# Optimization experiments

Measured on AMD Instinct MI355X. Metric: run time of the kernel, lower is better.

The kernel has to match this reference:

```python
import jax, jax.numpy as jnp
import numpy as np

N = 50000      # nodes
E = 800000     # edges (avg degree 16)
IN = 128       # in_feats
HID = 32       # hidden_feats per head
H = 4          # num_heads
NEG_SLOPE = 0.2


def setup_inputs() -> dict:
    key = jax.random.key(0)
    ks = jax.random.split(key, 13)
    x = jax.random.normal(ks[0], (N, IN), jnp.float32)
    src = jax.random.randint(ks[1], (E,), 0, N, jnp.int32)
    dst = jax.random.randint(ks[2], (E,), 0, N, jnp.int32)

    def lin(k, fi, fo):
        return jax.random.normal(k, (fi, fo), jnp.float32) * (1.0 / np.sqrt(fi))

    # conv1: IN -> H*HID
    W1 = lin(ks[3], IN, H * HID)
    al1 = jax.random.normal(ks[4], (H, HID), jnp.float32) * 0.1
    ar1 = jax.random.normal(ks[5], (H, HID), jnp.float32) * 0.1
    b1 = jnp.zeros((H, HID), jnp.float32)
    # conv2: H*HID -> H*HID
    W2 = lin(ks[6], H * HID, H * HID)
    al2 = jax.random.normal(ks[7], (H, HID), jnp.float32) * 0.1
    ar2 = jax.random.normal(ks[8], (H, HID), jnp.float32) * 0.1
    b2 = jnp.zeros((H, HID), jnp.float32)
    # fc: HID -> 1
    fcW = lin(ks[9], HID, 1)
    fcb = jnp.zeros((1,), jnp.float32)
    return {"x": x, "src": src, "dst": dst,
            "W1": W1, "al1": al1, "ar1": ar1, "b1": b1,
            "W2": W2, "al2": al2, "ar2": ar2, "b2": b2,
            "fcW": fcW, "fcb": fcb}


def gat_conv(x, src, dst, W, al, ar, b):
    # x: [N, F_in] -> feat: [N, H, HID]
    feat = (x @ W).reshape(N, H, HID)
    el = jnp.sum(feat * al, axis=-1)            # [N, H]
    er = jnp.sum(feat * ar, axis=-1)            # [N, H]
    e = jax.nn.leaky_relu(el[src] + er[dst], NEG_SLOPE)  # [E, H]
    # segment softmax over incoming edges of each dst node
    m = jax.ops.segment_max(e, dst, num_segments=N)      # [N, H]
    ex = jnp.exp(e - m[dst])                              # [E, H]
    denom = jax.ops.segment_sum(ex, dst, num_segments=N)  # [N, H]
    alpha = ex / denom[dst]                                # [E, H]
    msg = feat[src] * alpha[:, :, None]                    # [E, H, HID]
    out = jax.ops.segment_sum(msg, dst, num_segments=N)   # [N, H, HID]
    return out + b[None, :, :]


def reference(x, src, dst, W1, al1, ar1, b1, W2, al2, ar2, b2, fcW, fcb):
    h = gat_conv(x, src, dst, W1, al1, ar1, b1).reshape(N, H * HID)
    h = jax.nn.relu(h)
    # dropout(0.5) is identity in eval mode
    h = gat_conv(h, src, dst, W2, al2, ar2, b2).mean(axis=1)  # [N, HID]
    return h @ fcW + fcb                                       # [N, 1]
```

## Files before the change

kernel.cpp:

```cpp
#include <hip/hip_runtime.h>
#include <hip/hip_fp16.h>

#define LEAK 0.2f
#define CAP 64

static __device__ inline unsigned pack_h2(float a, float b) {
    __half2 h = __floats2half2_rn(a, b);
    unsigned u; __builtin_memcpy(&u, &h, 4); return u;
}
static __device__ inline int swz(int c, int j) {
    int qb = j >> 3, r = j & 7;
    return c * 144 + qb * 8 + (qb >> 2) * 4 + r;
}
static __device__ inline unsigned q4(float4 v, float is) {
    int x0 = __float2int_rn(v.x * is) + 128; x0 = min(max(x0, 0), 255);
    int x1 = __float2int_rn(v.y * is) + 128; x1 = min(max(x1, 0), 255);
    int x2 = __float2int_rn(v.z * is) + 128; x2 = min(max(x2, 0), 255);
    int x3 = __float2int_rn(v.w * is) + 128; x3 = min(max(x3, 0), 255);
    return (unsigned)x0 | ((unsigned)x1 << 8) | ((unsigned)x2 << 16) | ((unsigned)x3 << 24);
}

__global__ __launch_bounds__(256, 4) void k1(
    const float* __restrict__ X, const float* __restrict__ W,
    const float* __restrict__ al, const float* __restrict__ ar,
    float2* __restrict__ elsc2, float* __restrict__ er_nh,
    unsigned* __restrict__ fq8,
    int* __restrict__ cnt,
    const float* __restrict__ W2, const float* __restrict__ al2,
    const float* __restrict__ ar2, const float* __restrict__ fcW,
    const float* __restrict__ b2, float* __restrict__ WfT,
    float* __restrict__ bc, int N, int ntiles, int zb) {
    __shared__ float sW[32 * 128];
    __shared__ float sXT[32 * 128];
    const int b = blockIdx.x;
    const int t = threadIdx.x;

    if (b >= ntiles) {
        int bb = b - ntiles;
        if (bb < zb) {
            int i = bb * 256 + t;
            if (i < N) cnt[i] = 0;
        } else {
            int idx = (bb - zb) * 256 + t;
            if (idx < 1536) {
                int c = idx >> 7, k = idx & 127;
                int h = c & 3, sel = c >> 2;
                const float* vec = (sel == 0) ? (al2 + 32 * h)
                                 : (sel == 1) ? (ar2 + 32 * h) : fcW;
                float s = 0.f;
#pragma unroll 8
                for (int m = 0; m < 32; m++) s += W2[k * 128 + 32 * h + m] * vec[m];
                WfT[c * 128 + k] = s;
            } else if (idx < 1540) {
                int h = idx - 1536;
                float s = 0.f;
                for (int m = 0; m < 32; m++) s += b2[h * 32 + m] * fcW[m];
                bc[h] = s;
            }
        }
        return;
    }

    const int r0 = b * 128;
    const int tx = t & 15;
    const int ty = t >> 4;
    const float4* X4 = (const float4*)X;
    const float4* W4 = (const float4*)W;
    float4* sW4 = (float4*)sW;
    const float4* sXT4 = (const float4*)sXT;

    float4 acc[8][2];
#pragma unroll
    for (int r = 0; r < 8; r++) {
        acc[r][0] = make_float4(0.f, 0.f, 0.f, 0.f);
        acc[r][1] = make_float4(0.f, 0.f, 0.f, 0.f);
    }
    for (int ks = 0; ks < 4; ++ks) {
        if (ks) __syncthreads();
#pragma unroll
        for (int i = 0; i < 4; i++) {
            int idx = i * 256 + t;
            sW4[idx] = W4[1024 * ks + idx];
        }
#pragma unroll
        for (int i = 0; i < 4; i++) {
            int idx = i * 256 + t;
            int row = idx >> 3;
            int kq = idx & 7;
            float4 v = make_float4(0.f, 0.f, 0.f, 0.f);
            if (r0 + row < N) v = X4[(size_t)(r0 + row) * 32 + ks * 8 + kq];
            int sc = (((row >> 2) ^ kq)) * 4 + (row & 3);
            sXT[(4 * kq + 0) * 128 + sc] = v.x;
            sXT[(4 * kq + 1) * 128 + sc] = v.y;
            sXT[(4 * kq + 2) * 128 + sc] = v.z;
            sXT[(4 * kq + 3) * 128 + sc] = v.w;
        }
        __syncthreads();
#pragma unroll 4
        for (int k = 0; k < 32; k++) {
            float4 w0 = sW4[k * 32 + tx];
            float4 w1 = sW4[k * 32 + 16 + tx];
            float4 x0 = sXT4[k * 32 + (ty ^ (k >> 2))];
            float4 x1 = sXT4[k * 32 + ((16 + ty) ^ (k >> 2))];
            float xs[8] = {x0.x, x0.y, x0.z, x0.w, x1.x, x1.y, x1.z, x1.w};
#pragma unroll
            for (int r = 0; r < 8; r++) {
                acc[r][0].x += xs[r] * w0.x; acc[r][0].y += xs[r] * w0.y;
                acc[r][0].z += xs[r] * w0.z; acc[r][0].w += xs[r] * w0.w;
                acc[r][1].x += xs[r] * w1.x; acc[r][1].y += xs[r] * w1.y;
                acc[r][1].z += xs[r] * w1.z; acc[r][1].w += xs[r] * w1.w;
            }
        }
    }
    const float4* al4p = (const float4*)al;
    const float4* ar4p = (const float4*)ar;
    float4 alA = al4p[tx], alB = al4p[16 + tx];
    float4 arA = ar4p[tx], arB = ar4p[16 + tx];
#pragma unroll
    for (int r = 0; r < 8; r++) {
        int lrow = (r < 4) ? (ty * 4 + r) : (64 + ty * 4 + (r - 4));
        int row = r0 + lrow;
        bool ok = row < N;
        float4 a0 = acc[r][0], a1 = acc[r][1];
        float m = fmaxf(fmaxf(fmaxf(fabsf(a0.x), fabsf(a0.y)),
                              fmaxf(fabsf(a0.z), fabsf(a0.w))),
                        fmaxf(fmaxf(fabsf(a1.x), fabsf(a1.y)),
                              fmaxf(fabsf(a1.z), fabsf(a1.w))));
#pragma unroll
        for (int off = 1; off < 16; off <<= 1) m = fmaxf(m, __shfl_xor(m, off));
        float scale = m * (1.f / 127.f);
        float is = (m > 0.f) ? (127.f / m) : 0.f;
        if (ok) {
            fq8[(size_t)row * 32 + tx] = q4(a0, is);
            fq8[(size_t)row * 32 + 16 + tx] = q4(a1, is);
        }
        float elA = a0.x * alA.x + a0.y * alA.y + a0.z * alA.z + a0.w * alA.w;
        float erA = a0.x * arA.x + a0.y * arA.y + a0.z * arA.z + a0.w * arA.w;
        float elB = a1.x * alB.x + a1.y * alB.y + a1.z * alB.z + a1.w * alB.w;
        float erB = a1.x * arB.x + a1.y * arB.y + a1.z * arB.z + a1.w * arB.w;
#pragma unroll
        for (int off = 1; off < 8; off <<= 1) {
            elA += __shfl_xor(elA, off); erA += __shfl_xor(erA, off);
            elB += __shfl_xor(elB, off); erB += __shfl_xor(erB, off);
        }
        if (ok && tx == 0) {
            elsc2[row * 4 + 0] = make_float2(elA, scale);
            elsc2[row * 4 + 2] = make_float2(elB, scale);
            er_nh[row * 4 + 0] = erA;
            er_nh[row * 4 + 2] = erB;
        }
        if (ok && tx == 8) {
            elsc2[row * 4 + 1] = make_float2(elA, scale);
            elsc2[row * 4 + 3] = make_float2(elB, scale);
            er_nh[row * 4 + 1] = erA;
            er_nh[row * 4 + 3] = erB;
        }
    }
}

__global__ __launch_bounds__(256) void k_ell(
    const int* __restrict__ src, const int* __restrict__ dst,
    int* __restrict__ cnt, unsigned short* __restrict__ ell,
    int E, int N, int R) {
    const int part = blockIdx.x & 7;
    const int rank = blockIdx.x >> 3;
    const int S = (N + 7) >> 3;
    const int lo = part * S;
    const int hi = (lo + S < N) ? (lo + S) : N;
    const int per = (E + R - 1) / R;
    const int e0 = rank * per;
    const int e1 = (e0 + per < E) ? (e0 + per) : E;
    for (int e = e0 + threadIdx.x; e < e1; e += 256) {
        int d = dst[e];
        if (d >= lo && d < hi) {
            int s = src[e];
            int pos = atomicAdd(&cnt[d], 1);
            if (pos < CAP) ell[(size_t)d * CAP + pos] = (unsigned short)s;
        }
    }
}

__global__ __launch_bounds__(256) void k_agg1P(
    const unsigned* __restrict__ fq8, const float2* __restrict__ elsc2,
    const float* __restrict__ er_nh, const unsigned short* __restrict__ ell,
    const int* __restrict__ cnt, const float* __restrict__ b1,
    const float* __restrict__ WfT, float2* __restrict__ Pag,
    float* __restrict__ er2, int N) {
    __shared__ float sWf[12 * 144];
    for (int i = threadIdx.x; i < 1536; i += 256)
        sWf[swz(i >> 7, i & 127)] = WfT[i];
    __syncthreads();
    const int wave = threadIdx.x >> 6, lane = threadIdx.x & 63;
    const int nsub = lane >> 4, q = lane & 15, h = q >> 2;
    const int wbase = q * 8 + (q >> 2) * 4;
    const uint2* fq2 = (const uint2*)fq8;

    const int n = blockIdx.x * 16 + wave * 4 + nsub;
    const bool nok = n < N;
    const int nc = nok ? n : (N - 1);
    int deg = nok ? cnt[n] : 0; if (deg > CAP) deg = CAP;
    float er = nok ? er_nh[n * 4 + h] : 0.f;
    const unsigned short* row = ell + (size_t)nc * CAP;

    int dm = deg;
    dm = max(dm, __shfl_xor(dm, 16));
    dm = max(dm, __shfl_xor(dm, 32));

    float acc[8] = {0.f, 0.f, 0.f, 0.f, 0.f, 0.f, 0.f, 0.f};
    float den = 0.f, wss = 0.f;
    for (int jt = 0; jt < dm; jt += 16) {
        int s_all = (jt + q < CAP) ? (int)row[jt + q] : 0;
        int lim = dm - jt; if (lim > 16) lim = 16;
        for (int u = 0; u < lim; u += 8) {
            int sv[8]; float2 esv[8]; uint2 fv[8];
#pragma unroll
            for (int v = 0; v < 8; v++) {
                int jj = jt + u + v;
                int s = __shfl(s_all, (lane & 48) | ((u + v) & 15));
                sv[v] = (jj < deg) ? s : 0;
            }
#pragma unroll
            for (int v = 0; v < 8; v++) esv[v] = elsc2[sv[v] * 4 + h];
#pragma unroll
            for (int v = 0; v < 8; v++) fv[v] = fq2[(size_t)sv[v] * 16 + q];
#pragma unroll
            for (int v = 0; v < 8; v++) {
                int jj = jt + u + v;
                bool valid = jj < deg;
                float e = esv[v].x + er;
                e = fmaxf(e, LEAK * e);
                float w = valid ? __expf(e) : 0.f;
                float ws = w * esv[v].y;
                unsigned ua = fv[v].x, ub = fv[v].y;
                acc[0] += ws * (float)(ua & 0xff);
                acc[1] += ws * (float)((ua >> 8) & 0xff);
                acc[2] += ws * (float)((ua >> 16) & 0xff);
                acc[3] += ws * (float)(ua >> 24);
                acc[4] += ws * (float)(ub & 0xff);
                acc[5] += ws * (float)((ub >> 8) & 0xff);
                acc[6] += ws * (float)((ub >> 16) & 0xff);
                acc[7] += ws * (float)(ub >> 24);
                den += w; wss += ws;
            }
        }
    }
    float inv = (den > 0.f) ? (1.f / den) : 0.f;
    float off128 = 128.f * wss;
    float4 b1a = ((const float4*)b1)[q * 2];
    float4 b1b = ((const float4*)b1)[q * 2 + 1];
    float hv[8];
    hv[0] = fmaxf((acc[0] - off128) * inv + b1a.x, 0.f);
    hv[1] = fmaxf((acc[1] - off128) * inv + b1a.y, 0.f);
    hv[2] = fmaxf((acc[2] - off128) * inv + b1a.z, 0.f);
    hv[3] = fmaxf((acc[3] - off128) * inv + b1a.w, 0.f);
    hv[4] = fmaxf((acc[4] - off128) * inv + b1b.x, 0.f);
    hv[5] = fmaxf((acc[5] - off128) * inv + b1b.y, 0.f);
    hv[6] = fmaxf((acc[6] - off128) * inv + b1b.z, 0.f);
    hv[7] = fmaxf((acc[7] - off128) * inv + b1b.w, 0.f);
    float p[12];
#pragma unroll
    for (int c = 0; c < 12; c++) {
        const float* wr = sWf + c * 144 + wbase;
        float4 wa = *(const float4*)wr;
        float4 wb = *(const float4*)(wr + 4);
        p[c] = hv[0] * wa.x + hv[1] * wa.y + hv[2] * wa.z + hv[3] * wa.w
             + hv[4] * wb.x + hv[5] * wb.y + hv[6] * wb.z + hv[7] * wb.w;
    }
#pragma unroll
    for (int off = 1; off < 16; off <<= 1) {
#pragma unroll
        for (int c = 0; c < 12; c++) p[c] += __shfl_xor(p[c], off);
    }
    if (nok) {
        if (q < 4) Pag[(size_t)n * 4 + q] = make_float2(p[q], p[8 + q]);
        else if (q < 8) er2[(size_t)n * 4 + (q - 4)] = p[q];
    }
}

__global__ __launch_bounds__(256) void k_agg2(
    const float2* __restrict__ Pag, const float* __restrict__ er2,
    const unsigned short* __restrict__ ell, const int* __restrict__ cnt,
    const float* __restrict__ bc, const float* __restrict__ fcb,
    float* __restrict__ out, int N) {
    int idx = blockIdx.x * 256 + threadIdx.x;
    int n = idx >> 2, h = idx & 3;
    if (n >= N) return;
    int deg = cnt[n]; if (deg > CAP) deg = CAP;
    float er = er2[(size_t)n * 4 + h];
    const unsigned short* row = ell + (size_t)n * CAP;
    float num = 0.f, den = 0.f;
    int j = 0, d4 = deg & ~3;
    for (; j < d4; j += 4) {
        ushort4 ss = *(const ushort4*)(row + j);
        int s0 = ss.x, s1 = ss.y, s2 = ss.z, s3 = ss.w;
        float2 g0 = Pag[(size_t)s0 * 4 + h];
        float2 g1 = Pag[(size_t)s1 * 4 + h];
        float2 g2 = Pag[(size_t)s2 * 4 + h];
        float2 g3 = Pag[(size_t)s3 * 4 + h];
        float e0 = g0.x + er; e0 = fmaxf(e0, LEAK * e0); float w0 = __expf(e0);
        float e1 = g1.x + er; e1 = fmaxf(e1, LEAK * e1); float w1 = __expf(e1);
        float e2 = g2.x + er; e2 = fmaxf(e2, LEAK * e2); float w2 = __expf(e2);
        float e3 = g3.x + er; e3 = fmaxf(e3, LEAK * e3); float w3 = __expf(e3);
        num += w0 * g0.y + w1 * g1.y + w2 * g2.y + w3 * g3.y;
        den += (w0 + w1) + (w2 + w3);
    }
    for (; j < deg; ++j) {
        int s = row[j];
        float2 gg = Pag[(size_t)s * 4 + h];
        float e = gg.x + er; e = fmaxf(e, LEAK * e);
        float w = __expf(e);
        num += w * gg.y; den += w;
    }
    float r = (den > 0.f) ? (num / den) : 0.f;
    r += bc[h];
    r += __shfl_xor(r, 1);
    r += __shfl_xor(r, 2);
    if (h == 0) out[n] = 0.25f * r + fcb[0];
}

extern "C" void kernel_launch(void* const* d_in, const int* in_sizes, int n_in,
                              void* d_out, int out_size, void* d_ws, size_t ws_size,
                              hipStream_t stream) {
    const float* x   = (const float*)d_in[0];
    const int* src   = (const int*)d_in[1];
    const int* dst   = (const int*)d_in[2];
    const float* W1  = (const float*)d_in[3];
    const float* al1 = (const float*)d_in[4];
    const float* ar1 = (const float*)d_in[5];
    const float* b1  = (const float*)d_in[6];
    const float* W2  = (const float*)d_in[7];
    const float* al2 = (const float*)d_in[8];
    const float* ar2 = (const float*)d_in[9];
    const float* b2  = (const float*)d_in[10];
    const float* fcW = (const float*)d_in[11];
    const float* fcb = (const float*)d_in[12];
    float* out = (float*)d_out;

    const int N = in_sizes[0] / 128;
    const int E = in_sizes[1];

    char* w = (char*)d_ws;
    size_t off = 0;
    auto alloc = [&](size_t bytes) {
        void* p = w + off;
        off = (off + bytes + 255) & ~(size_t)255;
        return p;
    };
    unsigned* fq8  = (unsigned*)alloc((size_t)N * 32 * 4);
    float2* elsc2  = (float2*)alloc((size_t)N * 4 * 8);
    float* er_nh   = (float*)alloc((size_t)N * 4 * 4);
    float2* Pag    = (float2*)alloc((size_t)N * 4 * 8);
    float* er2     = (float*)alloc((size_t)N * 4 * 4);
    float* WfT     = (float*)alloc((size_t)(12 * 128 + 4) * 4);
    float* bc      = WfT + 12 * 128;
    int* cnt       = (int*)alloc((size_t)N * 4);
    unsigned short* ell = (unsigned short*)alloc((size_t)N * CAP * 2);

    const int zb = (N + 255) / 256;
    const int ntiles = (N + 127) / 128;
    const int R = 256;

    k1<<<ntiles + zb + 8, 256, 0, stream>>>(
        x, W1, al1, ar1, elsc2, er_nh, fq8,
        cnt, W2, al2, ar2, fcW, b2, WfT, bc, N, ntiles, zb);
    k_ell<<<8 * R, 256, 0, stream>>>(src, dst, cnt, ell, E, N, R);
    k_agg1P<<<(N + 15) / 16, 256, 0, stream>>>(
        fq8, elsc2, er_nh, ell, cnt, b1, WfT, Pag, er2, N);
    k_agg2<<<(N * 4 + 255) / 256, 256, 0, stream>>>(
        Pag, er2, ell, cnt, bc, fcb, out, N);
}
```

Before: 204.8 us.

## Pad per-node degree counters to 64 bytes and unroll agg2 gather by 8

Spreads each node's atomic degree counter onto its own 64-byte slot so concurrent atomicAdds from different nodes no longer contend on shared cache lines. The zeroing pass now clears the larger counter array with int4 stores. Separately, the k_agg2 neighbour loop is unrolled to 8 with all gathers issued before the math, giving more loads in flight. The k1 occupancy hint is raised from 4 to 5 blocks per SM. The costs are a 16x larger counter buffer, scattered strided reads of deg in the aggregation kernels, and more register pressure in k1 and k_agg2.

Result: slower. 267.3 us (+30.5%).

```diff
diff --git a/kernel.cpp b/kernel.cpp
--- a/kernel.cpp
+++ b/kernel.cpp
@@ -3,11 +3,8 @@
 
 #define LEAK 0.2f
 #define CAP 64
-
-static __device__ inline unsigned pack_h2(float a, float b) {
-    __half2 h = __floats2half2_rn(a, b);
-    unsigned u; __builtin_memcpy(&u, &h, 4); return u;
-}
+#define CS 16
+
 static __device__ inline int swz(int c, int j) {
     int qb = j >> 3, r = j & 7;
     return c * 144 + qb * 8 + (qb >> 2) * 4 + r;
@@ -20,7 +17,7 @@
     return (unsigned)x0 | ((unsigned)x1 << 8) | ((unsigned)x2 << 16) | ((unsigned)x3 << 24);
 }
 
-__global__ __launch_bounds__(256, 4) void k1(
+__global__ __launch_bounds__(256, 5) void k1(
     const float* __restrict__ X, const float* __restrict__ W,
     const float* __restrict__ al, const float* __restrict__ ar,
     float2* __restrict__ elsc2, float* __restrict__ er_nh,
@@ -39,7 +36,9 @@
         int bb = b - ntiles;
         if (bb < zb) {
             int i = bb * 256 + t;
-            if (i < N) cnt[i] = 0;
+            if (i < N * (CS / 4)) {
+                ((int4*)cnt)[i] = make_int4(0, 0, 0, 0);
+            }
         } else {
             int idx = (bb - zb) * 256 + t;
             if (idx < 1536) {
@@ -174,7 +173,7 @@
         int d = dst[e];
         if (d >= lo && d < hi) {
             int s = src[e];
-            int pos = atomicAdd(&cnt[d], 1);
+            int pos = atomicAdd(&cnt[d * CS], 1);
             if (pos < CAP) ell[(size_t)d * CAP + pos] = (unsigned short)s;
         }
     }
@@ -198,7 +197,7 @@
     const int n = blockIdx.x * 16 + wave * 4 + nsub;
     const bool nok = n < N;
     const int nc = nok ? n : (N - 1);
-    int deg = nok ? cnt[n] : 0; if (deg > CAP) deg = CAP;
+    int deg = nok ? cnt[n * CS] : 0; if (deg > CAP) deg = CAP;
     float er = nok ? er_nh[n * 4 + h] : 0.f;
     const unsigned short* row = ell + (size_t)nc * CAP;
 
@@ -285,24 +284,24 @@
     int idx = blockIdx.x * 256 + threadIdx.x;
     int n = idx >> 2, h = idx & 3;
     if (n >= N) return;
-    int deg = cnt[n]; if (deg > CAP) deg = CAP;
+    int deg = cnt[n * CS]; if (deg > CAP) deg = CAP;
     float er = er2[(size_t)n * 4 + h];
     const unsigned short* row = ell + (size_t)n * CAP;
     float num = 0.f, den = 0.f;
-    int j = 0, d4 = deg & ~3;
-    for (; j < d4; j += 4) {
-        ushort4 ss = *(const ushort4*)(row + j);
-        int s0 = ss.x, s1 = ss.y, s2 = ss.z, s3 = ss.w;
-        float2 g0 = Pag[(size_t)s0 * 4 + h];
-        float2 g1 = Pag[(size_t)s1 * 4 + h];
-        float2 g2 = Pag[(size_t)s2 * 4 + h];
-        float2 g3 = Pag[(size_t)s3 * 4 + h];
-        float e0 = g0.x + er; e0 = fmaxf(e0, LEAK * e0); float w0 = __expf(e0);
-        float e1 = g1.x + er; e1 = fmaxf(e1, LEAK * e1); float w1 = __expf(e1);
-        float e2 = g2.x + er; e2 = fmaxf(e2, LEAK * e2); float w2 = __expf(e2);
-        float e3 = g3.x + er; e3 = fmaxf(e3, LEAK * e3); float w3 = __expf(e3);
-        num += w0 * g0.y + w1 * g1.y + w2 * g2.y + w3 * g3.y;
-        den += (w0 + w1) + (w2 + w3);
+    int j = 0, d8 = deg & ~7;
+    for (; j < d8; j += 8) {
+        ushort4 sa = *(const ushort4*)(row + j);
+        ushort4 sb = *(const ushort4*)(row + j + 4);
+        int sv[8] = {sa.x, sa.y, sa.z, sa.w, sb.x, sb.y, sb.z, sb.w};
+        float2 g[8];
+#pragma unroll
+        for (int v = 0; v < 8; v++) g[v] = Pag[(size_t)sv[v] * 4 + h];
+#pragma unroll
+        for (int v = 0; v < 8; v++) {
+            float e = g[v].x + er; e = fmaxf(e, LEAK * e);
+            float w = __expf(e);
+            num += w * g[v].y; den += w;
+        }
     }
     for (; j < deg; ++j) {
         int s = row[j];
@@ -353,10 +352,10 @@
     float* er2     = (float*)alloc((size_t)N * 4 * 4);
     float* WfT     = (float*)alloc((size_t)(12 * 128 + 4) * 4);
     float* bc      = WfT + 12 * 128;
-    int* cnt       = (int*)alloc((size_t)N * 4);
+    int* cnt       = (int*)alloc((size_t)N * CS * 4);
     unsigned short* ell = (unsigned short*)alloc((size_t)N * CAP * 2);
 
-    const int zb = (N + 255) / 256;
+    const int zb = (N * (CS / 4) + 255) / 256;
     const int ntiles = (N + 127) / 128;
     const int R = 256;
 
```
